# Optimization experiments

Hardware: AMD Instinct MI355X
Metric: run time of the kernel (lower is better)

## Reference

```python
import jax, jax.numpy as jnp
import numpy as np

N_HITS = 16384
N_EDGES = 262144
N_GROUPS = 512
N_EVENTS = 64
IN_CH = 25
HID = 128
HEADS = 4
DH = HID // HEADS
LAYERS = 3
EDGE_DIM = 5
FFN = 4 * HID
EPS = 1e-5


def setup_inputs() -> dict:
    key = jax.random.key(0)
    ks = jax.random.split(key, 16)
    def nrm(k, shape, s=0.05):
        return jax.random.normal(k, shape, dtype=jnp.float32) * s
    z = lambda *s: jnp.zeros(s, jnp.float32)
    return {
        "x": jax.random.normal(ks[0], (N_HITS, IN_CH), dtype=jnp.float32),
        "edge_index": jax.random.randint(ks[1], (2, N_EDGES), 0, N_HITS, dtype=jnp.int32),
        "edge_attr": jax.random.normal(ks[2], (N_EDGES, EDGE_DIM), dtype=jnp.float32),
        "group_indices": jax.random.randint(ks[3], (N_HITS,), 0, N_GROUPS, dtype=jnp.int32),
        "batch_indices_per_group": jnp.sort(jax.random.randint(ks[4], (N_GROUPS,), 0, N_EVENTS, dtype=jnp.int32)),
        "embed_W": nrm(ks[5], (IN_CH, HID)),
        "embed_b": z(HID),
        "blk_Wqkv": nrm(ks[6], (LAYERS, HID, 3 * HID)),
        "blk_bqkv": z(LAYERS, 3 * HID),
        "blk_We": nrm(ks[7], (LAYERS, EDGE_DIM, HID)),
        "blk_be": z(LAYERS, HID),
        "blk_Wo": nrm(ks[8], (LAYERS, HID, HID)),
        "blk_bo": z(LAYERS, HID),
        "ln1_g": jnp.ones((LAYERS, HID), jnp.float32),
        "ln1_b": z(LAYERS, HID),
        "ffn_W1": nrm(ks[9], (LAYERS, HID, FFN)),
        "ffn_b1": z(LAYERS, FFN),
        "ffn_W2": nrm(ks[10], (LAYERS, FFN, HID)),
        "ffn_b2": z(LAYERS, HID),
        "ln2_g": jnp.ones((LAYERS, HID), jnp.float32),
        "ln2_b": z(LAYERS, HID),
        "aff_W1": nrm(ks[11], (4 * HID, HID)),
        "aff_b1": z(HID),
        "aff_W2": nrm(ks[12], (HID, 1)),
        "aff_b2": z(1),
    }


def _layer_norm(v, g, b):
    mu = jnp.mean(v, axis=-1, keepdims=True)
    var = jnp.mean((v - mu) ** 2, axis=-1, keepdims=True)
    return (v - mu) * jax.lax.rsqrt(var + EPS) * g + b


def reference(x, edge_index, edge_attr, group_indices, batch_indices_per_group,
              embed_W, embed_b, blk_Wqkv, blk_bqkv, blk_We, blk_be, blk_Wo, blk_bo,
              ln1_g, ln1_b, ffn_W1, ffn_b1, ffn_W2, ffn_b2, ln2_g, ln2_b,
              aff_W1, aff_b1, aff_W2, aff_b2):
    n = x.shape[0]
    G = batch_indices_per_group.shape[0]
    src, dst = edge_index[0], edge_index[1]
    scale = 1.0 / np.sqrt(DH).astype(np.float32)

    h = x @ embed_W + embed_b  # [N, HID]
    for l in range(LAYERS):
        # edge-conditioned multi-head attention over the graph edges
        qkv = h @ blk_Wqkv[l] + blk_bqkv[l]
        q, k, v = jnp.split(qkv, 3, axis=-1)
        e = edge_attr @ blk_We[l] + blk_be[l]          # [E, HID]
        qe = q[dst].reshape(-1, HEADS, DH)              # [E, h, d]
        ke = (k[src] + e).reshape(-1, HEADS, DH)
        ve = (v[src] + e).reshape(-1, HEADS, DH)
        logits = jnp.einsum("ehd,ehd->eh", qe, ke) * scale
        m = jax.ops.segment_max(logits, dst, num_segments=n)
        m = jnp.where(jnp.isfinite(m), m, 0.0)          # nodes with no in-edges
        p = jnp.exp(logits - m[dst])
        s = jax.ops.segment_sum(p, dst, num_segments=n)
        attn = jax.ops.segment_sum(p[:, :, None] * ve, dst, num_segments=n)
        attn = (attn / jnp.maximum(s, 1e-9)[:, :, None]).reshape(n, HID)
        h = _layer_norm(h + attn @ blk_Wo[l] + blk_bo[l], ln1_g[l], ln1_b[l])
        f = jax.nn.relu(h @ ffn_W1[l] + ffn_b1[l]) @ ffn_W2[l] + ffn_b2[l]
        h = _layer_norm(h + f, ln2_g[l], ln2_b[l])

    # group pooling (multi-scatter)
    raw_view = x[:, 3].astype(jnp.int32)  # truncation, matches torch .long()
    cnt_all = jax.ops.segment_sum(jnp.ones((n,), jnp.float32), group_indices, num_segments=G)
    g_max = jax.ops.segment_max(h, group_indices, num_segments=G)
    g_max = jnp.where(cnt_all[:, None] > 0, g_max, 0.0)  # torch_scatter fills empty with 0

    def pool_view(view_id):
        w = (raw_view == view_id).astype(jnp.float32)
        cnt = jax.ops.segment_sum(w, group_indices, num_segments=G)
        summ = jax.ops.segment_sum(h * w[:, None], group_indices, num_segments=G)
        pooled = summ / jnp.maximum(cnt, 1.0)[:, None]
        has = (cnt > 0).astype(jnp.float32)[:, None]
        return pooled, has

    pool_x, has_x = pool_view(0)
    pool_y, has_y = pool_view(1)
    sum_feat = pool_x * has_x + pool_y * has_y
    valid = jnp.maximum(has_x + has_y, 1.0)
    ge = jnp.concatenate([sum_feat / valid, g_max], axis=1)  # [G, 2*HID]

    # pairwise affinity MLP: Linear(4H->H) split so the [G,G,4H] concat is never built
    W1a, W1b = aff_W1[: 2 * HID], aff_W1[2 * HID:]
    pre = (ge @ W1a)[:, None, :] + (ge @ W1b)[None, :, :] + aff_b1  # [G, G, HID]
    scores = (jax.nn.relu(pre) @ aff_W2 + aff_b2)[..., 0]           # [G, G]
    scores = 0.5 * (scores + scores.T)
    event_mask = batch_indices_per_group[:, None] == batch_indices_per_group[None, :]
    return jax.nn.sigmoid(scores) * event_mask.astype(scores.dtype)
```

## Files before the change

### kernel.cpp

```cpp
#include <hip/hip_runtime.h>
#include <hip/hip_bf16.h>

#define NHITS   16384
#define NEDGES  262144
#define NGROUPS 512
#define HID     128
#define LAYERS  3
#define FFND    512
#define MAXDEG  64
#define GCAP    96

typedef __attribute__((ext_vector_type(8))) short bf16x8;
typedef __attribute__((ext_vector_type(8))) unsigned short ushort8;
typedef __attribute__((ext_vector_type(4))) float floatx4;

__device__ __forceinline__ float bf2f(ushort u) {
    return __uint_as_float(((unsigned)u) << 16);
}
__device__ __forceinline__ ushort f2bf(float f) {
    unsigned u = __float_as_uint(f);
    unsigned r = (u + 0x7FFFu + ((u >> 16) & 1u)) >> 16;
    return (ushort)r;
}

__device__ __forceinline__ void gl2lds16(const ushort* gp, ushort* lp) {
    __builtin_amdgcn_global_load_lds(
        (const __attribute__((address_space(1))) unsigned int*)(gp),
        (__attribute__((address_space(3))) unsigned int*)(lp), 16, 0, 0);
}


struct TD { const float* src; ushort* dst; int K; int N; };
struct TDs { TD d[14]; };

__global__ __launch_bounds__(256) void transpose_all(TDs tds, int* __restrict__ zbuf,
                                                     int ztotal) {
    __shared__ float lds[32][33];
    if (blockIdx.y == 0) {
        for (int gz = blockIdx.x * 256 + threadIdx.x; gz < ztotal; gz += 64 * 256)
            zbuf[gz] = 0;
    }
    TD d = tds.d[blockIdx.y];
    int tX = d.N >> 5;
    int tiles = (d.K >> 5) * tX;
    if ((int)blockIdx.x >= tiles) return;
    int tk = blockIdx.x / tX, tn = blockIdx.x % tX;
    int k0 = tk * 32, n0 = tn * 32;
    int r = threadIdx.x >> 5, c = threadIdx.x & 31;
#pragma unroll
    for (int i = 0; i < 4; ++i)
        lds[r + i * 8][c] = d.src[(size_t)(k0 + r + i * 8) * d.N + n0 + c];
    __syncthreads();
#pragma unroll
    for (int i = 0; i < 4; ++i) {
        int n = n0 + r + i * 8;
        d.dst[(size_t)n * d.K + k0 + c] = f2bf(lds[c][r + i * 8]);
    }
}


__global__ __launch_bounds__(256) void scatter_embed(
        const int* __restrict__ src, const int* __restrict__ dst,
        const float* __restrict__ ea, const int* __restrict__ gidx,
        int* __restrict__ cnt, int* __restrict__ cnt2,
        int* __restrict__ ps, float* __restrict__ pea, int* __restrict__ hlist,
        const float* __restrict__ x, const float* __restrict__ embW,
        const float* __restrict__ embB, float* __restrict__ h,
        ushort* __restrict__ hb) {
    const int vb = blockIdx.x, t = threadIdx.x;
    if (vb < 1024) {
        int e = vb * 256 + t;
        int d = dst[e];
        int slot = atomicAdd(&cnt[d], 1);
        if (slot < MAXDEG) {
            size_t pos = (size_t)d * MAXDEG + slot;
            ps[pos] = src[e];
#pragma unroll
            for (int j = 0; j < 5; ++j) pea[pos * 5 + j] = ea[(size_t)e * 5 + j];
        }
        if (e < NHITS) {
            int g = gidx[e];
            int slot2 = atomicAdd(&cnt2[g], 1);
            if (slot2 < GCAP) hlist[g * GCAP + slot2] = e;
        }
    } else {
        __shared__ float xs[2][32];
        int base = (vb - 1024) * 32;
        for (int it = 0; it < 16; ++it) {
            int i0 = base + it * 2;
            __syncthreads();
            if (t < 25) xs[0][t] = x[(size_t)i0 * 25 + t];
            else if (t >= 128 && t < 153) xs[1][t - 128] = x[(size_t)(i0 + 1) * 25 + (t - 128)];
            __syncthreads();
            int node = i0 + (t >> 7), c = t & 127;
            const float* xr = xs[t >> 7];
            float s = embB[c];
#pragma unroll
            for (int k = 0; k < 25; ++k) s += xr[k] * embW[k * HID + c];
            h[(size_t)node * HID + c] = s;
            hb[(size_t)node * HID + c] = f2bf(s);
        }
    }
}


__global__ __launch_bounds__(256) void gemm_mfma_k(const ushort* __restrict__ A,
                                                   const ushort* __restrict__ Bt,
                                                   const float* __restrict__ bias,
                                                   ushort* __restrict__ C,
                                                   int N, int K, int relu) {
    __shared__ ushort As[128 * 32];
    __shared__ ushort Bs[128 * 32];
    const int t = threadIdx.x;
    const int lane = t & 63;
    const int w = t >> 6;
    const int wr = w >> 1, wc = w & 1;
    const int lm = lane & 15, q = lane >> 4;
    const int row0 = blockIdx.y * 128;
    const int col0 = blockIdx.x * 128;
    const int sr = t >> 2, sc = (t & 3) * 8;
    const int sr2 = (t + 256) >> 2, sc2 = ((t + 256) & 3) * 8;

    floatx4 acc[4][4] = {};
    for (int k0 = 0; k0 < K; k0 += 32) {
        gl2lds16(A + (size_t)(row0 + sr) * K + k0 + sc,   &As[t * 8]);
        gl2lds16(A + (size_t)(row0 + sr2) * K + k0 + sc2, &As[t * 8 + 2048]);
        gl2lds16(Bt + (size_t)(col0 + sr) * K + k0 + sc,   &Bs[t * 8]);
        gl2lds16(Bt + (size_t)(col0 + sr2) * K + k0 + sc2, &Bs[t * 8 + 2048]);
        __syncthreads();
        bf16x8 af[4], bf[4];
#pragma unroll
        for (int it = 0; it < 4; ++it)
            af[it] = *(const bf16x8*)&As[(wr * 64 + it * 16 + lm) * 32 + q * 8];
#pragma unroll
        for (int jt = 0; jt < 4; ++jt)
            bf[jt] = *(const bf16x8*)&Bs[(wc * 64 + jt * 16 + lm) * 32 + q * 8];
#pragma unroll
        for (int it = 0; it < 4; ++it)
#pragma unroll
            for (int jt = 0; jt < 4; ++jt)
                acc[it][jt] = __builtin_amdgcn_mfma_f32_16x16x32_bf16(
                    af[it], bf[jt], acc[it][jt], 0, 0, 0);
        __syncthreads();
    }
#pragma unroll
    for (int jt = 0; jt < 4; ++jt) {
        int col = col0 + wc * 64 + jt * 16 + lm;
        float bb = bias ? bias[col] : 0.f;
#pragma unroll
        for (int it = 0; it < 4; ++it)
#pragma unroll
            for (int r = 0; r < 4; ++r) {
                int row = row0 + wr * 64 + it * 16 + q * 4 + r;
                float o = acc[it][jt][r] + bb;
                if (relu) o = fmaxf(o, 0.f);
                C[(size_t)row * N + col] = f2bf(o);
            }
    }
}


__global__ __launch_bounds__(256) void attnwo_k(
        const ushort* __restrict__ qkv, const int* __restrict__ ps,
        const float* __restrict__ pea, const int* __restrict__ cnt,
        const float* __restrict__ We, const float* __restrict__ be,
        const ushort* __restrict__ Wot, const float* __restrict__ bo,
        const float* __restrict__ g, const float* __restrict__ b,
        float* __restrict__ h, ushort* __restrict__ hb) {
    __shared__ float WeS[640], beS[128];
    __shared__ ushort As[32 * 136];
    __shared__ ushort Bs[128 * 32];
    __shared__ float redS[64], redQ[64];
    const int t = threadIdx.x;
    for (int idx = t; idx < 640; idx += 256) WeS[idx] = We[idx];
    if (t < 128) beS[t] = be[t];
    __syncthreads();
    const int row0 = blockIdx.x * 32;
    const int w = t >> 6, lane = t & 63;
    const int grp = lane >> 4, cb = (lane & 15) * 8;
    const float scale = 0.17677669529663687f;

    for (int n = 0; n < 8; ++n) {
        const int i = row0 + w * 8 + n;
        float qv[8];
        {
            ushort8 qq = *(const ushort8*)(qkv + (size_t)i * 384 + cb);
#pragma unroll
            for (int j = 0; j < 8; ++j) qv[j] = bf2f(qq[j]);
        }
        float pj[6];
#pragma unroll
        for (int k = 0; k < 5; ++k) {
            float s = 0.f;
#pragma unroll
            for (int j = 0; j < 8; ++j) s += qv[j] * WeS[k * 128 + cb + j];
            pj[k] = s;
        }
        {
            float sb = 0.f;
#pragma unroll
            for (int j = 0; j < 8; ++j) sb += qv[j] * beS[cb + j];
            pj[5] = sb;
        }
#pragma unroll
        for (int k = 0; k < 6; ++k) {
            pj[k] += __shfl_xor(pj[k], 1);
            pj[k] += __shfl_xor(pj[k], 2);
        }
        float S = 0.f, T0 = 0.f, T1 = 0.f, T2 = 0.f, T3 = 0.f, T4 = 0.f;
        float acc[8] = {};
        const int endc = min(cnt[i], MAXDEG);
        const size_t pbase = (size_t)i * MAXDEG;
#pragma unroll 2
        for (int p0 = 0; p0 < endc; p0 += 4) {
            int pp = p0 + grp;
            bool act = pp < endc;
            int slot = act ? pp : (endc - 1);
            int s = ps[pbase + slot];
            const float* eap = pea + (pbase + slot) * 5;
            float a0 = eap[0], a1 = eap[1], a2 = eap[2], a3 = eap[3], a4 = eap[4];
            const ushort* srow = qkv + (size_t)s * 384;
            ushort8 kk = *(const ushort8*)(srow + 128 + cb);
            ushort8 vv = *(const ushort8*)(srow + 256 + cb);
            float part = 0.f;
#pragma unroll
            for (int j = 0; j < 8; ++j) part += qv[j] * bf2f(kk[j]);
            part += __shfl_xor(part, 1);
            part += __shfl_xor(part, 2);
            float logit = (part + pj[5] + a0 * pj[0] + a1 * pj[1] + a2 * pj[2]
                           + a3 * pj[3] + a4 * pj[4]) * scale;
            float pe = act ? __expf(logit) : 0.f;
            S += pe;
            T0 += pe * a0; T1 += pe * a1; T2 += pe * a2; T3 += pe * a3; T4 += pe * a4;
#pragma unroll
            for (int j = 0; j < 8; ++j) acc[j] += pe * bf2f(vv[j]);
        }
#pragma unroll
        for (int j = 0; j < 8; ++j) {
            acc[j] += __shfl_xor(acc[j], 16);
            acc[j] += __shfl_xor(acc[j], 32);
        }
        S += __shfl_xor(S, 16);   S += __shfl_xor(S, 32);
        T0 += __shfl_xor(T0, 16); T0 += __shfl_xor(T0, 32);
        T1 += __shfl_xor(T1, 16); T1 += __shfl_xor(T1, 32);
        T2 += __shfl_xor(T2, 16); T2 += __shfl_xor(T2, 32);
        T3 += __shfl_xor(T3, 16); T3 += __shfl_xor(T3, 32);
        T4 += __shfl_xor(T4, 16); T4 += __shfl_xor(T4, 32);
        if (grp == 0) {
            float inv = 1.f / fmaxf(S, 1e-9f);
            ushort8 o;
#pragma unroll
            for (int j = 0; j < 8; ++j) {
                float wadd = WeS[cb + j] * T0 + WeS[128 + cb + j] * T1
                           + WeS[256 + cb + j] * T2 + WeS[384 + cb + j] * T3
                           + WeS[512 + cb + j] * T4 + beS[cb + j] * S;
                o[j] = f2bf((acc[j] + wadd) * inv);
            }
            *(ushort8*)&As[(w * 8 + n) * 136 + cb] = o;
        }
    }
    __syncthreads();

    const int wr = w >> 1, wc = w & 1;
    const int lm = lane & 15, q = lane >> 4;
    const int sr = t >> 2, sc = (t & 3) * 8;
    const int sr2 = (t + 256) >> 2, sc2 = ((t + 256) & 3) * 8;
    floatx4 acc2[4] = {};
    for (int k0 = 0; k0 < 128; k0 += 32) {
        gl2lds16(Wot + (size_t)sr * HID + k0 + sc,   &Bs[t * 8]);
        gl2lds16(Wot + (size_t)sr2 * HID + k0 + sc2, &Bs[t * 8 + 2048]);
        __syncthreads();
        bf16x8 af = *(const bf16x8*)&As[(wr * 16 + lm) * 136 + k0 + q * 8];
#pragma unroll
        for (int jt = 0; jt < 4; ++jt) {
            bf16x8 bf = *(const bf16x8*)&Bs[(wc * 64 + jt * 16 + lm) * 32 + q * 8];
            acc2[jt] = __builtin_amdgcn_mfma_f32_16x16x32_bf16(af, bf, acc2[jt], 0, 0, 0);
        }
        __syncthreads();
    }
    float psum[4] = {}, psq[4] = {};
#pragma unroll
    for (int jt = 0; jt < 4; ++jt) {
        int col = wc * 64 + jt * 16 + lm;
        float bb = bo[col];
#pragma unroll
        for (int r = 0; r < 4; ++r) {
            int row = row0 + wr * 16 + q * 4 + r;
            float v = acc2[jt][r] + bb + h[(size_t)row * HID + col];
            acc2[jt][r] = v;
            psum[r] += v;
            psq[r] += v * v;
        }
    }
#pragma unroll
    for (int r = 0; r < 4; ++r) {
        float s = psum[r], ss = psq[r];
#pragma unroll
        for (int k = 1; k < 16; k <<= 1) {
            s += __shfl_xor(s, k, 16);
            ss += __shfl_xor(ss, k, 16);
        }
        psum[r] = s; psq[r] = ss;
    }
    if (lm == 0)
#pragma unroll
        for (int r = 0; r < 4; ++r) {
            int rl = wr * 16 + q * 4 + r;
            redS[rl * 2 + wc] = psum[r];
            redQ[rl * 2 + wc] = psq[r];
        }
    __syncthreads();
#pragma unroll
    for (int r = 0; r < 4; ++r) {
        int rl = wr * 16 + q * 4 + r;
        float tot = redS[rl * 2] + redS[rl * 2 + 1];
        float totq = redQ[rl * 2] + redQ[rl * 2 + 1];
        float mu = tot * (1.f / HID);
        float var = totq * (1.f / HID) - mu * mu;
        float rstd = rsqrtf(var + 1e-5f);
        int row = row0 + rl;
#pragma unroll
        for (int jt = 0; jt < 4; ++jt) {
            int col = wc * 64 + jt * 16 + lm;
            float o = (acc2[jt][r] - mu) * rstd * g[col] + b[col];
            h[(size_t)row * HID + col] = o;
            hb[(size_t)row * HID + col] = f2bf(o);
        }
    }
}


__global__ __launch_bounds__(256) void ffn_k(const ushort* __restrict__ hbuf,
                                             const ushort* __restrict__ W1t,
                                             const float* __restrict__ b1v,
                                             const ushort* __restrict__ W2t,
                                             const float* __restrict__ b2v,
                                             const float* __restrict__ g,
                                             const float* __restrict__ b,
                                             float* __restrict__ h,
                                             ushort* __restrict__ hb) {
    __shared__ ushort As[32 * 136];
    __shared__ ushort Bs[128 * 32];
    __shared__ ushort mid[32 * 520];
    __shared__ float redS[64], redQ[64];
    const int t = threadIdx.x;
    const int lane = t & 63;
    const int w = t >> 6;
    const int wr = w >> 1, wc = w & 1;
    const int lm = lane & 15, q = lane >> 4;
    const int row0 = blockIdx.x * 32;
    const int sr = t >> 2, sc = (t & 3) * 8;
    const int sr2 = (t + 256) >> 2, sc2 = ((t + 256) & 3) * 8;

    for (int i = t; i < 32 * 16; i += 256) {
        int row = i >> 4, c8 = (i & 15) * 8;
        *(ushort8*)&As[row * 136 + c8] =
            *(const ushort8*)(hbuf + (size_t)(row0 + row) * HID + c8);
    }
    __syncthreads();

    for (int nc = 0; nc < 4; ++nc) {
        floatx4 acc1[4] = {};
        for (int k0 = 0; k0 < 128; k0 += 32) {
            gl2lds16(W1t + (size_t)(nc * 128 + sr) * HID + k0 + sc,   &Bs[t * 8]);
            gl2lds16(W1t + (size_t)(nc * 128 + sr2) * HID + k0 + sc2, &Bs[t * 8 + 2048]);
            __syncthreads();
            bf16x8 af = *(const bf16x8*)&As[(wr * 16 + lm) * 136 + k0 + q * 8];
#pragma unroll
            for (int jt = 0; jt < 4; ++jt) {
                bf16x8 bf = *(const bf16x8*)&Bs[(wc * 64 + jt * 16 + lm) * 32 + q * 8];
                acc1[jt] = __builtin_amdgcn_mfma_f32_16x16x32_bf16(af, bf, acc1[jt], 0, 0, 0);
            }
            __syncthreads();
        }
#pragma unroll
        for (int jt = 0; jt < 4; ++jt) {
            int col = wc * 64 + jt * 16 + lm;
            float bb = b1v[nc * 128 + col];
#pragma unroll
            for (int r = 0; r < 4; ++r) {
                int row = wr * 16 + q * 4 + r;
                mid[row * 520 + nc * 128 + col] = f2bf(fmaxf(acc1[jt][r] + bb, 0.f));
            }
        }
    }
    __syncthreads();

    floatx4 acc2[4] = {};
    for (int k0 = 0; k0 < 512; k0 += 32) {
        gl2lds16(W2t + (size_t)sr * FFND + k0 + sc,   &Bs[t * 8]);
        gl2lds16(W2t + (size_t)sr2 * FFND + k0 + sc2, &Bs[t * 8 + 2048]);
        __syncthreads();
        bf16x8 af = *(const bf16x8*)&mid[(wr * 16 + lm) * 520 + k0 + q * 8];
#pragma unroll
        for (int jt = 0; jt < 4; ++jt) {
            bf16x8 bf = *(const bf16x8*)&Bs[(wc * 64 + jt * 16 + lm) * 32 + q * 8];
            acc2[jt] = __builtin_amdgcn_mfma_f32_16x16x32_bf16(af, bf, acc2[jt], 0, 0, 0);
        }
        __syncthreads();
    }

    float psum[4] = {}, psq[4] = {};
#pragma unroll
    for (int jt = 0; jt < 4; ++jt) {
        int col = wc * 64 + jt * 16 + lm;
        float bb = b2v[col];
#pragma unroll
        for (int r = 0; r < 4; ++r) {
            int row = row0 + wr * 16 + q * 4 + r;
            float v = acc2[jt][r] + bb + h[(size_t)row * HID + col];
            acc2[jt][r] = v;
            psum[r] += v;
            psq[r] += v * v;
        }
    }
#pragma unroll
    for (int r = 0; r < 4; ++r) {
        float s = psum[r], ss = psq[r];
#pragma unroll
        for (int k = 1; k < 16; k <<= 1) {
            s += __shfl_xor(s, k, 16);
            ss += __shfl_xor(ss, k, 16);
        }
        psum[r] = s; psq[r] = ss;
    }
    if (lm == 0)
#pragma unroll
        for (int r = 0; r < 4; ++r) {
            int rl = wr * 16 + q * 4 + r;
            redS[rl * 2 + wc] = psum[r];
            redQ[rl * 2 + wc] = psq[r];
        }
    __syncthreads();
#pragma unroll
    for (int r = 0; r < 4; ++r) {
        int rl = wr * 16 + q * 4 + r;
        float tot = redS[rl * 2] + redS[rl * 2 + 1];
        float totq = redQ[rl * 2] + redQ[rl * 2 + 1];
        float mu = tot * (1.f / HID);
        float var = totq * (1.f / HID) - mu * mu;
        float rstd = rsqrtf(var + 1e-5f);
        int row = row0 + rl;
#pragma unroll
        for (int jt = 0; jt < 4; ++jt) {
            int col = wc * 64 + jt * 16 + lm;
            float o = (acc2[jt][r] - mu) * rstd * g[col] + b[col];
            h[(size_t)row * HID + col] = o;
            hb[(size_t)row * HID + col] = f2bf(o);
        }
    }
}


__global__ __launch_bounds__(128) void pool_group(const float* __restrict__ h,
                                                  const float* __restrict__ x,
                                                  const int* __restrict__ hlist,
                                                  const int* __restrict__ cnt2,
                                                  ushort* __restrict__ geb) {
    int g = blockIdx.x, c = threadIdx.x;
    int n = min(cnt2[g], GCAP);
    float mx = -INFINITY, sx = 0.f, sy = 0.f, cx = 0.f, cy = 0.f;
    for (int p = 0; p < n; ++p) {
        int i = hlist[g * GCAP + p];
        float hv = h[(size_t)i * HID + c];
        mx = fmaxf(mx, hv);
        int view = (int)x[(size_t)i * 25 + 3];
        if (view == 0) { sx += hv; cx += 1.f; }
        else if (view == 1) { sy += hv; cy += 1.f; }
    }
    float gm = (n > 0) ? mx : 0.f;
    float px = sx / fmaxf(cx, 1.f), py = sy / fmaxf(cy, 1.f);
    float hx = cx > 0.f ? 1.f : 0.f, hy = cy > 0.f ? 1.f : 0.f;
    float sf = px * hx + py * hy;
    float valid = fmaxf(hx + hy, 1.f);
    geb[g * 256 + c] = f2bf(sf / valid);
    geb[g * 256 + 128 + c] = f2bf(gm);
}


__global__ __launch_bounds__(256) void score_final(const ushort* __restrict__ Cab,
                                                   const float* __restrict__ W2,
                                                   const float* __restrict__ b1v,
                                                   const float* __restrict__ b2,
                                                   const int* __restrict__ ev,
                                                   float* __restrict__ out) {
    int bi = blockIdx.y, bj = blockIdx.x;
    if (bj < bi) return;
    __shared__ float Ai[16][129], Bi[16][129], Aj[16][129], Bj[16][129];
    __shared__ float w2s[128], b1s[128];
    int t = threadIdx.y * 16 + threadIdx.x;
    int i0 = bi * 16, j0 = bj * 16;
    for (int idx = t; idx < 2048; idx += 256) {
        int r = idx >> 7, k = idx & 127;
        Ai[r][k] = bf2f(Cab[(size_t)(i0 + r) * 256 + k]);
        Bi[r][k] = bf2f(Cab[(size_t)(i0 + r) * 256 + 128 + k]);
        Aj[r][k] = bf2f(Cab[(size_t)(j0 + r) * 256 + k]);
        Bj[r][k] = bf2f(Cab[(size_t)(j0 + r) * 256 + 128 + k]);
    }
    if (t < 128) { w2s[t] = W2[t]; b1s[t] = b1v[t]; }
    __syncthreads();
    int tx = threadIdx.x, ty = threadIdx.y;
    float sij = 0.f, sji = 0.f;
#pragma unroll 4
    for (int k = 0; k < 128; ++k) {
        float pb = b1s[k], wk = w2s[k];
        sij += fmaxf(Ai[ty][k] + Bj[tx][k] + pb, 0.f) * wk;
        sji += fmaxf(Aj[tx][k] + Bi[ty][k] + pb, 0.f) * wk;
    }
    float z = 0.5f * (sij + sji) + b2[0];
    float sg = 1.f / (1.f + __expf(-z));
    int gi = i0 + ty, gj = j0 + tx;
    float res = (ev[gi] == ev[gj]) ? sg : 0.f;
    out[(size_t)gi * NGROUPS + gj] = res;
    out[(size_t)gj * NGROUPS + gi] = res;
}


static inline char* align256(char* p) {
    return (char*)(((uintptr_t)p + 255) & ~(uintptr_t)255);
}

extern "C" void kernel_launch(void* const* d_in, const int* in_sizes, int n_in,
                              void* d_out, int out_size, void* d_ws, size_t ws_size,
                              hipStream_t stream) {
    const float* x    = (const float*)d_in[0];
    const int* eidx   = (const int*)d_in[1];
    const float* ea   = (const float*)d_in[2];
    const int* gidx   = (const int*)d_in[3];
    const int* ev     = (const int*)d_in[4];
    const float* embW = (const float*)d_in[5];
    const float* embB = (const float*)d_in[6];
    const float* Wqkv = (const float*)d_in[7];
    const float* bqkv = (const float*)d_in[8];
    const float* We   = (const float*)d_in[9];
    const float* be   = (const float*)d_in[10];
    const float* Wo   = (const float*)d_in[11];
    const float* bo   = (const float*)d_in[12];
    const float* ln1g = (const float*)d_in[13];
    const float* ln1b = (const float*)d_in[14];
    const float* W1   = (const float*)d_in[15];
    const float* b1   = (const float*)d_in[16];
    const float* W2   = (const float*)d_in[17];
    const float* b2   = (const float*)d_in[18];
    const float* ln2g = (const float*)d_in[19];
    const float* ln2b = (const float*)d_in[20];
    const float* affW1 = (const float*)d_in[21];
    const float* affb1 = (const float*)d_in[22];
    const float* affW2 = (const float*)d_in[23];
    const float* affb2 = (const float*)d_in[24];

    const int* src = eidx;
    const int* dst = eidx + NEDGES;

    char* p = (char*)d_ws;
    float* h    = (float*)p;            p += (size_t)NHITS * HID * 4;
    float* pea  = (float*)p;            p += (size_t)NHITS * MAXDEG * 5 * 4;
    int* cnt    = (int*)p;              p += NHITS * 4;
    int* cnt2   = (int*)p;              p += NGROUPS * 4;
    int* ps     = (int*)p;              p += (size_t)NHITS * MAXDEG * 4;
    int* hlist  = (int*)p;              p += NGROUPS * GCAP * 4;
    p = align256(p);
    ushort* hb    = (ushort*)p;         p += (size_t)NHITS * HID * 2;
    ushort* qkvb  = (ushort*)p;         p += (size_t)NHITS * 384 * 2;
    ushort* geb   = (ushort*)p;         p += (size_t)NGROUPS * 256 * 2;
    ushort* Cab   = (ushort*)p;         p += (size_t)NGROUPS * 256 * 2;
    p = align256(p);
    ushort* Wqkvt = (ushort*)p;         p += (size_t)LAYERS * 384 * HID * 2;
    ushort* Wot   = (ushort*)p;         p += (size_t)LAYERS * HID * HID * 2;
    ushort* W1t   = (ushort*)p;         p += (size_t)LAYERS * FFND * HID * 2;
    ushort* W2t   = (ushort*)p;         p += (size_t)LAYERS * HID * FFND * 2;
    ushort* W1abt = (ushort*)p;         p += (size_t)256 * 256 * 2;

    TDs tds;
    for (int l = 0; l < LAYERS; ++l) {
        tds.d[l * 4 + 0] = { Wqkv + (size_t)l * HID * 384, Wqkvt + (size_t)l * 384 * HID, HID, 384 };
        tds.d[l * 4 + 1] = { Wo + (size_t)l * HID * HID,   Wot + (size_t)l * HID * HID,   HID, HID };
        tds.d[l * 4 + 2] = { W1 + (size_t)l * HID * FFND,  W1t + (size_t)l * FFND * HID,  HID, FFND };
        tds.d[l * 4 + 3] = { W2 + (size_t)l * FFND * HID,  W2t + (size_t)l * HID * FFND,  FFND, HID };
    }
    tds.d[12] = { affW1,             W1abt,             256, HID };
    tds.d[13] = { affW1 + 256 * HID, W1abt + 128 * 256, 256, HID };
    transpose_all<<<dim3(64, 14), 256, 0, stream>>>(tds, cnt, NHITS + NGROUPS);

    scatter_embed<<<1536, 256, 0, stream>>>(src, dst, ea, gidx, cnt, cnt2,
                                            ps, pea, hlist, x, embW, embB, h, hb);

    for (int l = 0; l < LAYERS; ++l) {
        gemm_mfma_k<<<dim3(3, NHITS / 128), 256, 0, stream>>>(
            hb, Wqkvt + (size_t)l * 384 * HID, bqkv + l * 384, qkvb, 384, HID, 0);
        attnwo_k<<<NHITS / 32, 256, 0, stream>>>(
            qkvb, ps, pea, cnt, We + (size_t)l * 5 * HID, be + l * HID,
            Wot + (size_t)l * HID * HID, bo + l * HID,
            ln1g + l * HID, ln1b + l * HID, h, hb);
        ffn_k<<<NHITS / 32, 256, 0, stream>>>(
            hb, W1t + (size_t)l * FFND * HID, b1 + l * FFND,
            W2t + (size_t)l * HID * FFND, b2 + l * HID,
            ln2g + l * HID, ln2b + l * HID, h, hb);
    }

    pool_group<<<NGROUPS, 128, 0, stream>>>(h, x, hlist, cnt2, geb);
    gemm_mfma_k<<<dim3(2, NGROUPS / 128), 256, 0, stream>>>(
        geb, W1abt, nullptr, Cab, 256, 256, 0);
    score_final<<<dim3(NGROUPS / 16, NGROUPS / 16), dim3(16, 16), 0, stream>>>(
        Cab, affW2, affb1, affb2, ev, (float*)d_out);
}
```

Before: 407.9 us.

## Split fused attention+Wo kernel into per-node attention and separate GEMM+LayerNorm

```diff
diff --git a/kernel.cpp b/kernel.cpp
--- a/kernel.cpp
+++ b/kernel.cpp
@@ -160,134 +160,150 @@
 }
 
 
-__global__ __launch_bounds__(256) void attnwo_k(
-        const ushort* __restrict__ qkv, const int* __restrict__ ps,
-        const float* __restrict__ pea, const int* __restrict__ cnt,
-        const float* __restrict__ We, const float* __restrict__ be,
-        const ushort* __restrict__ Wot, const float* __restrict__ bo,
-        const float* __restrict__ g, const float* __restrict__ b,
-        float* __restrict__ h, ushort* __restrict__ hb) {
+__global__ __launch_bounds__(256) void attn_kernel(const ushort* __restrict__ qkv,
+                                                   const int* __restrict__ ps,
+                                                   const float* __restrict__ pea,
+                                                   const int* __restrict__ cnt,
+                                                   const float* __restrict__ We,
+                                                   const float* __restrict__ be,
+                                                   ushort* __restrict__ attnb) {
     __shared__ float WeS[640], beS[128];
-    __shared__ ushort As[32 * 136];
+    int t = threadIdx.x;
+    for (int idx = t; idx < 640; idx += 256) WeS[idx] = We[idx];
+    if (t < 128) beS[t] = be[t];
+    __syncthreads();
+    const int i = blockIdx.x * 4 + (t >> 6);
+    const int lane = t & 63;
+    const int grp = lane >> 4;
+    const int cb = (lane & 15) * 8;
+    float qv[8];
+    {
+        ushort8 qq = *(const ushort8*)(qkv + (size_t)i * 384 + cb);
+#pragma unroll
+        for (int j = 0; j < 8; ++j) qv[j] = bf2f(qq[j]);
+    }
+    float pj[6];
+#pragma unroll
+    for (int k = 0; k < 5; ++k) {
+        float s = 0.f;
+#pragma unroll
+        for (int j = 0; j < 8; ++j) s += qv[j] * WeS[k * 128 + cb + j];
+        pj[k] = s;
+    }
+    {
+        float sb = 0.f;
+#pragma unroll
+        for (int j = 0; j < 8; ++j) sb += qv[j] * beS[cb + j];
+        pj[5] = sb;
+    }
+#pragma unroll
+    for (int k = 0; k < 6; ++k) {
+        pj[k] += __shfl_xor(pj[k], 1);
+        pj[k] += __shfl_xor(pj[k], 2);
+    }
+    float S = 0.f, T0 = 0.f, T1 = 0.f, T2 = 0.f, T3 = 0.f, T4 = 0.f;
+    float acc[8] = {};
+    const int endc = min(cnt[i], MAXDEG);
+    const size_t pbase = (size_t)i * MAXDEG;
+    const float scale = 0.17677669529663687f;
+
+#pragma unroll 4
+    for (int p0 = 0; p0 < endc; p0 += 4) {
+        int pp = p0 + grp;
+        bool act = pp < endc;
+        int slot = act ? pp : (endc - 1);
+        int s = ps[pbase + slot];
+        const float* eap = pea + (pbase + slot) * 5;
+        float a0 = eap[0], a1 = eap[1], a2 = eap[2], a3 = eap[3], a4 = eap[4];
+        const ushort* srow = qkv + (size_t)s * 384;
+        ushort8 kk = *(const ushort8*)(srow + 128 + cb);
+        ushort8 vv = *(const ushort8*)(srow + 256 + cb);
+        float part = 0.f;
+#pragma unroll
+        for (int j = 0; j < 8; ++j) part += qv[j] * bf2f(kk[j]);
+        part += __shfl_xor(part, 1);
+        part += __shfl_xor(part, 2);
+        float logit = (part + pj[5] + a0 * pj[0] + a1 * pj[1] + a2 * pj[2]
+                       + a3 * pj[3] + a4 * pj[4]) * scale;
+        float pe = act ? __expf(logit) : 0.f;
+        S += pe;
+        T0 += pe * a0; T1 += pe * a1; T2 += pe * a2; T3 += pe * a3; T4 += pe * a4;
+#pragma unroll
+        for (int j = 0; j < 8; ++j) acc[j] += pe * bf2f(vv[j]);
+    }
+#pragma unroll
+    for (int j = 0; j < 8; ++j) {
+        acc[j] += __shfl_xor(acc[j], 16);
+        acc[j] += __shfl_xor(acc[j], 32);
+    }
+    S += __shfl_xor(S, 16);   S += __shfl_xor(S, 32);
+    T0 += __shfl_xor(T0, 16); T0 += __shfl_xor(T0, 32);
+    T1 += __shfl_xor(T1, 16); T1 += __shfl_xor(T1, 32);
+    T2 += __shfl_xor(T2, 16); T2 += __shfl_xor(T2, 32);
+    T3 += __shfl_xor(T3, 16); T3 += __shfl_xor(T3, 32);
+    T4 += __shfl_xor(T4, 16); T4 += __shfl_xor(T4, 32);
+    if (grp == 0) {
+        float inv = 1.f / fmaxf(S, 1e-9f);
+        ushort8 o;
+#pragma unroll
+        for (int j = 0; j < 8; ++j) {
+            float wadd = WeS[cb + j] * T0 + WeS[128 + cb + j] * T1
+                       + WeS[256 + cb + j] * T2 + WeS[384 + cb + j] * T3
+                       + WeS[512 + cb + j] * T4 + beS[cb + j] * S;
+            o[j] = f2bf((acc[j] + wadd) * inv);
+        }
+        *(ushort8*)(attnb + (size_t)i * HID + cb) = o;
+    }
+}
+
+
+__global__ __launch_bounds__(256) void gemm_ln_k(const ushort* __restrict__ A,
+                                                 const ushort* __restrict__ Bt,
+                                                 const float* __restrict__ bias,
+                                                 const float* __restrict__ g,
+                                                 const float* __restrict__ b,
+                                                 float* __restrict__ h,
+                                                 ushort* __restrict__ hb,
+                                                 int K) {
+    __shared__ ushort As[32 * 32];
     __shared__ ushort Bs[128 * 32];
     __shared__ float redS[64], redQ[64];
     const int t = threadIdx.x;
-    for (int idx = t; idx < 640; idx += 256) WeS[idx] = We[idx];
-    if (t < 128) beS[t] = be[t];
-    __syncthreads();
-    const int row0 = blockIdx.x * 32;
-    const int w = t >> 6, lane = t & 63;
-    const int grp = lane >> 4, cb = (lane & 15) * 8;
-    const float scale = 0.17677669529663687f;
-
-    for (int n = 0; n < 8; ++n) {
-        const int i = row0 + w * 8 + n;
-        float qv[8];
-        {
-            ushort8 qq = *(const ushort8*)(qkv + (size_t)i * 384 + cb);
-#pragma unroll
-            for (int j = 0; j < 8; ++j) qv[j] = bf2f(qq[j]);
-        }
-        float pj[6];
-#pragma unroll
-        for (int k = 0; k < 5; ++k) {
-            float s = 0.f;
-#pragma unroll
-            for (int j = 0; j < 8; ++j) s += qv[j] * WeS[k * 128 + cb + j];
-            pj[k] = s;
-        }
-        {
-            float sb = 0.f;
-#pragma unroll
-            for (int j = 0; j < 8; ++j) sb += qv[j] * beS[cb + j];
-            pj[5] = sb;
-        }
-#pragma unroll
-        for (int k = 0; k < 6; ++k) {
-            pj[k] += __shfl_xor(pj[k], 1);
-            pj[k] += __shfl_xor(pj[k], 2);
-        }
-        float S = 0.f, T0 = 0.f, T1 = 0.f, T2 = 0.f, T3 = 0.f, T4 = 0.f;
-        float acc[8] = {};
-        const int endc = min(cnt[i], MAXDEG);
-        const size_t pbase = (size_t)i * MAXDEG;
-#pragma unroll 2
-        for (int p0 = 0; p0 < endc; p0 += 4) {
-            int pp = p0 + grp;
-            bool act = pp < endc;
-            int slot = act ? pp : (endc - 1);
-            int s = ps[pbase + slot];
-            const float* eap = pea + (pbase + slot) * 5;
-            float a0 = eap[0], a1 = eap[1], a2 = eap[2], a3 = eap[3], a4 = eap[4];
-            const ushort* srow = qkv + (size_t)s * 384;
-            ushort8 kk = *(const ushort8*)(srow + 128 + cb);
-            ushort8 vv = *(const ushort8*)(srow + 256 + cb);
-            float part = 0.f;
-#pragma unroll
-            for (int j = 0; j < 8; ++j) part += qv[j] * bf2f(kk[j]);
-            part += __shfl_xor(part, 1);
-            part += __shfl_xor(part, 2);
-            float logit = (part + pj[5] + a0 * pj[0] + a1 * pj[1] + a2 * pj[2]
-                           + a3 * pj[3] + a4 * pj[4]) * scale;
-            float pe = act ? __expf(logit) : 0.f;
-            S += pe;
-            T0 += pe * a0; T1 += pe * a1; T2 += pe * a2; T3 += pe * a3; T4 += pe * a4;
-#pragma unroll
-            for (int j = 0; j < 8; ++j) acc[j] += pe * bf2f(vv[j]);
-        }
-#pragma unroll
-        for (int j = 0; j < 8; ++j) {
-            acc[j] += __shfl_xor(acc[j], 16);
-            acc[j] += __shfl_xor(acc[j], 32);
-        }
-        S += __shfl_xor(S, 16);   S += __shfl_xor(S, 32);
-        T0 += __shfl_xor(T0, 16); T0 += __shfl_xor(T0, 32);
-        T1 += __shfl_xor(T1, 16); T1 += __shfl_xor(T1, 32);
-        T2 += __shfl_xor(T2, 16); T2 += __shfl_xor(T2, 32);
-        T3 += __shfl_xor(T3, 16); T3 += __shfl_xor(T3, 32);
-        T4 += __shfl_xor(T4, 16); T4 += __shfl_xor(T4, 32);
-        if (grp == 0) {
-            float inv = 1.f / fmaxf(S, 1e-9f);
-            ushort8 o;
-#pragma unroll
-            for (int j = 0; j < 8; ++j) {
-                float wadd = WeS[cb + j] * T0 + WeS[128 + cb + j] * T1
-                           + WeS[256 + cb + j] * T2 + WeS[384 + cb + j] * T3
-                           + WeS[512 + cb + j] * T4 + beS[cb + j] * S;
-                o[j] = f2bf((acc[j] + wadd) * inv);
-            }
-            *(ushort8*)&As[(w * 8 + n) * 136 + cb] = o;
-        }
-    }
-    __syncthreads();
-
+    const int lane = t & 63;
+    const int w = t >> 6;
     const int wr = w >> 1, wc = w & 1;
     const int lm = lane & 15, q = lane >> 4;
+    const int row0 = blockIdx.x * 32;
     const int sr = t >> 2, sc = (t & 3) * 8;
     const int sr2 = (t + 256) >> 2, sc2 = ((t + 256) & 3) * 8;
-    floatx4 acc2[4] = {};
-    for (int k0 = 0; k0 < 128; k0 += 32) {
-        gl2lds16(Wot + (size_t)sr * HID + k0 + sc,   &Bs[t * 8]);
-        gl2lds16(Wot + (size_t)sr2 * HID + k0 + sc2, &Bs[t * 8 + 2048]);
+
+    floatx4 acc[4] = {};
+    for (int k0 = 0; k0 < K; k0 += 32) {
+        if (t < 128)
+            gl2lds16(A + (size_t)(row0 + sr) * K + k0 + sc, &As[t * 8]);
+        gl2lds16(Bt + (size_t)sr * K + k0 + sc,   &Bs[t * 8]);
+        gl2lds16(Bt + (size_t)sr2 * K + k0 + sc2, &Bs[t * 8 + 2048]);
         __syncthreads();
-        bf16x8 af = *(const bf16x8*)&As[(wr * 16 + lm) * 136 + k0 + q * 8];
-#pragma unroll
-        for (int jt = 0; jt < 4; ++jt) {
-            bf16x8 bf = *(const bf16x8*)&Bs[(wc * 64 + jt * 16 + lm) * 32 + q * 8];
-            acc2[jt] = __builtin_amdgcn_mfma_f32_16x16x32_bf16(af, bf, acc2[jt], 0, 0, 0);
-        }
+        bf16x8 af = *(const bf16x8*)&As[(wr * 16 + lm) * 32 + q * 8];
+        bf16x8 bf[4];
+#pragma unroll
+        for (int jt = 0; jt < 4; ++jt)
+            bf[jt] = *(const bf16x8*)&Bs[(wc * 64 + jt * 16 + lm) * 32 + q * 8];
+#pragma unroll
+        for (int jt = 0; jt < 4; ++jt)
+            acc[jt] = __builtin_amdgcn_mfma_f32_16x16x32_bf16(af, bf[jt], acc[jt], 0, 0, 0);
         __syncthreads();
     }
     float psum[4] = {}, psq[4] = {};
 #pragma unroll
     for (int jt = 0; jt < 4; ++jt) {
         int col = wc * 64 + jt * 16 + lm;
-        float bb = bo[col];
+        float bb = bias[col];
 #pragma unroll
         for (int r = 0; r < 4; ++r) {
             int row = row0 + wr * 16 + q * 4 + r;
-            float v = acc2[jt][r] + bb + h[(size_t)row * HID + col];
-            acc2[jt][r] = v;
+            float v = acc[jt][r] + bb + h[(size_t)row * HID + col];
+            acc[jt][r] = v;
             psum[r] += v;
             psq[r] += v * v;
         }
@@ -322,7 +338,7 @@
 #pragma unroll
         for (int jt = 0; jt < 4; ++jt) {
             int col = wc * 64 + jt * 16 + lm;
-            float o = (acc2[jt][r] - mu) * rstd * g[col] + b[col];
+            float o = (acc[jt][r] - mu) * rstd * g[col] + b[col];
             h[(size_t)row * HID + col] = o;
             hb[(size_t)row * HID + col] = f2bf(o);
         }
@@ -562,6 +578,7 @@
     p = align256(p);
     ushort* hb    = (ushort*)p;         p += (size_t)NHITS * HID * 2;
     ushort* qkvb  = (ushort*)p;         p += (size_t)NHITS * 384 * 2;
+    ushort* attnb = (ushort*)p;         p += (size_t)NHITS * HID * 2;
     ushort* geb   = (ushort*)p;         p += (size_t)NGROUPS * 256 * 2;
     ushort* Cab   = (ushort*)p;         p += (size_t)NGROUPS * 256 * 2;
     p = align256(p);
@@ -588,10 +605,11 @@
     for (int l = 0; l < LAYERS; ++l) {
         gemm_mfma_k<<<dim3(3, NHITS / 128), 256, 0, stream>>>(
             hb, Wqkvt + (size_t)l * 384 * HID, bqkv + l * 384, qkvb, 384, HID, 0);
-        attnwo_k<<<NHITS / 32, 256, 0, stream>>>(
-            qkvb, ps, pea, cnt, We + (size_t)l * 5 * HID, be + l * HID,
-            Wot + (size_t)l * HID * HID, bo + l * HID,
-            ln1g + l * HID, ln1b + l * HID, h, hb);
+        attn_kernel<<<NHITS / 4, 256, 0, stream>>>(
+            qkvb, ps, pea, cnt, We + (size_t)l * 5 * HID, be + l * HID, attnb);
+        gemm_ln_k<<<NHITS / 32, 256, 0, stream>>>(
+            attnb, Wot + (size_t)l * HID * HID, bo + l * HID,
+            ln1g + l * HID, ln1b + l * HID, h, hb, HID);
         ffn_k<<<NHITS / 32, 256, 0, stream>>>(
             hb, W1t + (size_t)l * FFND * HID, b1 + l * FFND,
             W2t + (size_t)l * HID * FFND, b2 + l * HID,
```

After: 373.2 us. 1.09x faster.
